# Kernel tuning notes

Measured on AMD Instinct MI355X. Metric: run time of the kernel, lower is better.

## Reference

```python
import jax, jax.numpy as jnp
import numpy as np

ZONEOUT = 0.15  # deterministic (eval-mode) zoneout on the output gate
HIDDEN = 128


def setup_inputs() -> dict:
    key = jax.random.key(0)
    k1, k2, k3, k4 = jax.random.split(key, 4)
    B, T, D, H = 512, 256, 256, HIDDEN
    x = jax.random.normal(k1, (B, T, D), dtype=jnp.float32)
    # gate projection for [i, f, o, g] gates, fan-in scaled
    Wx = jax.random.normal(k2, (4 * H, D), dtype=jnp.float32) / np.sqrt(D)
    Wh = jax.random.normal(k3, (4 * H, H), dtype=jnp.float32) / np.sqrt(H)
    b = jax.random.normal(k4, (4 * H,), dtype=jnp.float32) * 0.01
    return {"x": x, "Wx": Wx, "Wh": Wh, "b": b}


def reference(x, Wx, Wh, b):
    # x: [B, T, D]; returns (hids, cels, pogs) each [B, T, H]
    B, T, D = x.shape
    H = Wh.shape[1]
    z = jnp.asarray(ZONEOUT, dtype=x.dtype)

    def step(carry, xt):
        hid, cel, pog = carry  # each [B, H]
        gates = xt @ Wx.T + hid @ Wh.T + b  # [B, 4H]
        i_pre, f_pre, o_pre, g_pre = jnp.split(gates, 4, axis=-1)
        i = jax.nn.sigmoid(i_pre)
        f = jax.nn.sigmoid(f_pre)
        g = jnp.tanh(g_pre)
        # zoneout on the output gate: blend with previous output gate
        o = (1.0 - z) * jax.nn.sigmoid(o_pre) + z * pog
        cel_new = f * cel + i * g
        hid_new = o * jnp.tanh(cel_new)
        return (hid_new, cel_new, o), (hid_new, cel_new, o)

    zeros = jnp.zeros((B, H), dtype=x.dtype)
    xs = jnp.swapaxes(x, 0, 1)  # [T, B, D]
    _, (hids, cels, pogs) = jax.lax.scan(step, (zeros, zeros, zeros), xs)
    # [T, B, H] -> [B, T, H]
    return (jnp.swapaxes(hids, 0, 1), jnp.swapaxes(cels, 0, 1), jnp.swapaxes(pogs, 0, 1))
```

## Files before the change

### kernel.cpp

```cpp
#include <hip/hip_runtime.h>

typedef __attribute__((ext_vector_type(8))) short     bf16x8;
typedef __attribute__((ext_vector_type(4))) float     f32x4;

#define BSZ   512
#define TSZ   256
#define DSZ   256
#define HSZ   128
#define G4    512
#define OUT1  16777216L

__device__ inline unsigned short f2bf(float f) {
  union { float f; unsigned int u; } v; v.f = f;
  unsigned int r = (v.u + 0x7FFFu + ((v.u >> 16) & 1u)) >> 16;
  return (unsigned short)r;
}
__device__ inline float bf2f(unsigned int s) {
  union { unsigned int u; float f; } v; v.u = s << 16;
  return v.f;
}
__device__ inline float sig_fast(float x)  { return 1.0f / (1.0f + __expf(-x)); }
__device__ inline float tanh_fast(float x) { return 1.0f - 2.0f / (__expf(2.0f * x) + 1.0f); }

__global__ __launch_bounds__(512, 2)
void gemm_xw(const float* __restrict__ x, const float* __restrict__ Wx,
             const float* __restrict__ bias, unsigned short* __restrict__ xw) {
  __shared__ unsigned short aT[2][4096];

  const int tid = threadIdx.x;
  const int w   = tid >> 6;
  const int l   = tid & 63;
  const int p   = l & 15;
  const int r16 = l >> 4;
  const long m0blk = (long)blockIdx.x * 512;

  bf16x8 wf[4][8];
#pragma unroll
  for (int nt = 0; nt < 4; ++nt) {
#pragma unroll
    for (int c = 0; c < 8; ++c) {
      const float* src = Wx + (long)(w * 64 + nt * 16 + p) * DSZ + c * 32 + r16 * 8;
      float4 lo = *(const float4*)src;
      float4 hi = *(const float4*)(src + 4);
      bf16x8 f;
      f[0] = (short)f2bf(lo.x); f[1] = (short)f2bf(lo.y);
      f[2] = (short)f2bf(lo.z); f[3] = (short)f2bf(lo.w);
      f[4] = (short)f2bf(hi.x); f[5] = (short)f2bf(hi.y);
      f[6] = (short)f2bf(hi.z); f[7] = (short)f2bf(hi.w);
      wf[nt][c] = f;
    }
  }
  float bn[4];
#pragma unroll
  for (int nt = 0; nt < 4; ++nt) bn[nt] = bias[w * 64 + nt * 16 + p];

  const float* asrc = x + (m0blk + (l & 15)) * DSZ + (4 * w + r16) * 8;
  const int wl8 = (w * 64 + l) * 8;

  float4 va = *(const float4*)asrc;
  float4 vb = *(const float4*)(asrc + 4);
  asrc += 16 * DSZ;

  for (int i = 0; i < 32; ++i) {
    bf16x8 fr;
    fr[0] = (short)f2bf(va.x); fr[1] = (short)f2bf(va.y);
    fr[2] = (short)f2bf(va.z); fr[3] = (short)f2bf(va.w);
    fr[4] = (short)f2bf(vb.x); fr[5] = (short)f2bf(vb.y);
    fr[6] = (short)f2bf(vb.z); fr[7] = (short)f2bf(vb.w);
    *(bf16x8*)&aT[i & 1][wl8] = fr;

    if (i < 31) {
      va = *(const float4*)asrc;
      vb = *(const float4*)(asrc + 4);
      asrc += 16 * DSZ;
    }

    asm volatile("s_waitcnt lgkmcnt(0)" ::: "memory");
    __builtin_amdgcn_s_barrier();

    f32x4 acc[4];
#pragma unroll
    for (int nt = 0; nt < 4; ++nt)
      acc[nt] = (f32x4){bn[nt], bn[nt], bn[nt], bn[nt]};

#pragma unroll
    for (int c = 0; c < 8; ++c) {
      bf16x8 aF = *(const bf16x8*)&aT[i & 1][(c * 64 + l) * 8];
#pragma unroll
      for (int nt = 0; nt < 4; ++nt)
        acc[nt] = __builtin_amdgcn_mfma_f32_16x16x32_bf16(aF, wf[nt][c], acc[nt], 0, 0, 0);
    }

    const long rowbase = ((long)((i & 15) * 16 + r16 * 4) * BSZ + (blockIdx.x * 2 + (i >> 4))) * G4
                         + w * 64 + p;
#pragma unroll
    for (int r = 0; r < 4; ++r) {
      const long rb = rowbase + (long)r * (BSZ * G4);
#pragma unroll
      for (int nt = 0; nt < 4; ++nt)
        xw[rb + nt * 16] = f2bf(acc[nt][r]);
    }
  }
}

__global__ __launch_bounds__(512, 2)
void lstm_rec_mfma(const unsigned short* __restrict__ xw, const float* __restrict__ Wh,
                   float* __restrict__ outH, float* __restrict__ outC,
                   float* __restrict__ outP) {
  __shared__ unsigned short h_lds[2 * 2048];

  const int tid  = threadIdx.x;
  const int w    = tid >> 6;
  const int lane = tid & 63;
  const int p    = lane & 15;
  const int r16  = lane >> 4;
  const int b0   = blockIdx.x * 2;

  bf16x8 whF[4][4];
#pragma unroll
  for (int q = 0; q < 4; ++q) {
#pragma unroll
    for (int c = 0; c < 4; ++c) {
      const float* src = Wh + ((q * 128 + w * 16 + p) * HSZ + c * 32 + r16 * 8);
      float4 lo = *(const float4*)src;
      float4 hi = *(const float4*)(src + 4);
      bf16x8 f;
      f[0] = (short)f2bf(lo.x); f[1] = (short)f2bf(lo.y);
      f[2] = (short)f2bf(lo.z); f[3] = (short)f2bf(lo.w);
      f[4] = (short)f2bf(hi.x); f[5] = (short)f2bf(hi.y);
      f[6] = (short)f2bf(hi.z); f[7] = (short)f2bf(hi.w);
      whF[q][c] = f;
    }
  }

  for (int i = tid; i < 2 * 2048; i += 512) h_lds[i] = 0;

  float cel0 = 0.f, cel1 = 0.f, pog0 = 0.f, pog1 = 0.f;

  const int colw = w * 16 + p;
  const int c_  = colw >> 5, kk = colw & 31;
  const int lhi = (kk >> 3) << 4, jj = kk & 7;
  const int wr0 = c_ * 512 + (0 | lhi) * 8 + jj;
  const int wr1 = c_ * 512 + (1 | lhi) * 8 + jj;

  const unsigned short* xp = xw + (long)b0 * G4;
  const long XSTR = (long)BSZ * G4;

  unsigned int xvA[8], xvB[8];
#pragma unroll
  for (int q = 0; q < 4; ++q) {
    xvA[2 * q]     = xp[colw + q * 128];
    xvA[2 * q + 1] = xp[colw + G4 + q * 128];
  }
  xp += XSTR;

  float* pH0 = outH + (long)b0 * TSZ * HSZ;
  float* pC0 = outC + (long)b0 * TSZ * HSZ;
  float* pP0 = outP + (long)b0 * TSZ * HSZ;
  float* pH1 = pH0 + (long)TSZ * HSZ;
  float* pC1 = pC0 + (long)TSZ * HSZ;
  float* pP1 = pP0 + (long)TSZ * HSZ;

  f32x4 acc[4];
#pragma unroll
  for (int q = 0; q < 4; ++q) acc[q] = (f32x4){0.f, 0.f, 0.f, 0.f};

  __syncthreads();

#define STEP(RDOFF, WROFF, XC, XN, PREF)                                        \
  {                                                                             \
    bf16x8 aF[4];                                                               \
    _Pragma("unroll")                                                           \
    for (int c = 0; c < 4; ++c)                                                 \
      aF[c] = *(const bf16x8*)&h_lds[(RDOFF) + c * 512 + lane * 8];             \
    if (PREF) {                                                                 \
      _Pragma("unroll")                                                         \
      for (int q = 0; q < 4; ++q) {                                             \
        XN[2 * q]     = xp[colw + q * 128];                                     \
        XN[2 * q + 1] = xp[colw + G4 + q * 128];                                \
      }                                                                         \
      xp += XSTR;                                                               \
    }                                                                           \
    _Pragma("unroll")                                                           \
    for (int q = 0; q < 4; ++q) {                                               \
      acc[q][0] = bf2f(XC[2 * q]);                                              \
      acc[q][1] = bf2f(XC[2 * q + 1]);                                          \
    }                                                                           \
    _Pragma("unroll")                                                           \
    for (int q = 0; q < 4; ++q)                                                 \
      _Pragma("unroll")                                                         \
      for (int c = 0; c < 4; ++c)                                               \
        acc[q] = __builtin_amdgcn_mfma_f32_16x16x32_bf16(aF[c], whF[q][c], acc[q], 0, 0, 0); \
    float i0 = sig_fast(acc[0][0]), i1 = sig_fast(acc[0][1]);                   \
    float f0 = sig_fast(acc[1][0]), f1 = sig_fast(acc[1][1]);                   \
    float s0 = sig_fast(acc[2][0]), s1 = sig_fast(acc[2][1]);                   \
    float o0 = 0.85f * s0 + 0.15f * pog0, o1 = 0.85f * s1 + 0.15f * pog1;       \
    float g0 = tanh_fast(acc[3][0]), g1 = tanh_fast(acc[3][1]);                 \
    cel0 = f0 * cel0 + i0 * g0; cel1 = f1 * cel1 + i1 * g1;                     \
    float h0 = o0 * tanh_fast(cel0), h1 = o1 * tanh_fast(cel1);                 \
    pog0 = o0; pog1 = o1;                                                       \
    if (lane < 16) {                                                            \
      pH0[colw] = h0; pC0[colw] = cel0; pP0[colw] = o0;                         \
      pH1[colw] = h1; pC1[colw] = cel1; pP1[colw] = o1;                         \
      h_lds[(WROFF) + wr0] = f2bf(h0);                                          \
      h_lds[(WROFF) + wr1] = f2bf(h1);                                          \
    }                                                                           \
    pH0 += HSZ; pC0 += HSZ; pP0 += HSZ;                                         \
    pH1 += HSZ; pC1 += HSZ; pP1 += HSZ;                                         \
    asm volatile("s_waitcnt lgkmcnt(0)" ::: "memory");    \
    __builtin_amdgcn_s_barrier();                        \
  }

  for (int it = 0; it < 127; ++it) {
    STEP(0, 2048, xvA, xvB, true)
    STEP(2048, 0, xvB, xvA, true)
  }
  STEP(0, 2048, xvA, xvB, true)
  STEP(2048, 0, xvB, xvA, false)
#undef STEP
}

extern "C" void kernel_launch(void* const* d_in, const int* in_sizes, int n_in,
                              void* d_out, int out_size, void* d_ws, size_t ws_size,
                              hipStream_t stream) {
  const float* x    = (const float*)d_in[0];
  const float* Wx   = (const float*)d_in[1];
  const float* Wh   = (const float*)d_in[2];
  const float* bias = (const float*)d_in[3];

  float* outH = (float*)d_out;
  float* outC = outH + OUT1;
  float* outP = outC + OUT1;

  unsigned short* xwp = (unsigned short*)d_ws;

  dim3 g1(256), tb1(512);
  dim3 g2(256), tb2(512);

  gemm_xw<<<g1, tb1, 0, stream>>>(x, Wx, bias, xwp);
  lstm_rec_mfma<<<g2, tb2, 0, stream>>>(xwp, Wh, outH, outC, outP);
}
```

Measured before the change: 585.8 us.

## Process one batch row per recurrent block and interleave gate columns in xw

```diff
diff --git a/kernel.cpp b/kernel.cpp
--- a/kernel.cpp
+++ b/kernel.cpp
@@ -9,15 +9,18 @@
 #define HSZ   128
 #define G4    512
 #define OUT1  16777216L
+#define XSTR  262144L
 
 __device__ inline unsigned short f2bf(float f) {
   union { float f; unsigned int u; } v; v.f = f;
   unsigned int r = (v.u + 0x7FFFu + ((v.u >> 16) & 1u)) >> 16;
   return (unsigned short)r;
 }
-__device__ inline float bf2f(unsigned int s) {
-  union { unsigned int u; float f; } v; v.u = s << 16;
-  return v.f;
+__device__ inline float bf_lo(unsigned int u) {
+  union { unsigned int u; float f; } v; v.u = u << 16; return v.f;
+}
+__device__ inline float bf_hi(unsigned int u) {
+  union { unsigned int u; float f; } v; v.u = u & 0xFFFF0000u; return v.f;
 }
 __device__ inline float sig_fast(float x)  { return 1.0f / (1.0f + __expf(-x)); }
 __device__ inline float tanh_fast(float x) { return 1.0f - 2.0f / (__expf(2.0f * x) + 1.0f); }
@@ -91,19 +94,22 @@
         acc[nt] = __builtin_amdgcn_mfma_f32_16x16x32_bf16(aF, wf[nt][c], acc[nt], 0, 0, 0);
     }
 
-    const long rowbase = ((long)((i & 15) * 16 + r16 * 4) * BSZ + (blockIdx.x * 2 + (i >> 4))) * G4
-                         + w * 64 + p;
+    const int t0 = (i & 15) * 16 + r16 * 4;
+    const int bb = blockIdx.x * 2 + (i >> 4);
+    const int q  = w >> 1;
+    const int colw0 = (w & 1) * 64 + p;
+    const long base0 = (long)t0 * XSTR + (long)bb * G4 + colw0 * 4 + q;
 #pragma unroll
     for (int r = 0; r < 4; ++r) {
-      const long rb = rowbase + (long)r * (BSZ * G4);
+      const long rb = base0 + (long)r * XSTR;
 #pragma unroll
       for (int nt = 0; nt < 4; ++nt)
-        xw[rb + nt * 16] = f2bf(acc[nt][r]);
-    }
-  }
-}
-
-__global__ __launch_bounds__(512, 2)
+        xw[rb + nt * 64] = f2bf(acc[nt][r]);
+    }
+  }
+}
+
+__global__ __launch_bounds__(512, 4)
 void lstm_rec_mfma(const unsigned short* __restrict__ xw, const float* __restrict__ Wh,
                    float* __restrict__ outH, float* __restrict__ outC,
                    float* __restrict__ outP) {
@@ -114,7 +120,7 @@
   const int lane = tid & 63;
   const int p    = lane & 15;
   const int r16  = lane >> 4;
-  const int b0   = blockIdx.x * 2;
+  const int b    = blockIdx.x;
 
   bf16x8 whF[4][4];
 #pragma unroll
@@ -135,31 +141,22 @@
 
   for (int i = tid; i < 2 * 2048; i += 512) h_lds[i] = 0;
 
-  float cel0 = 0.f, cel1 = 0.f, pog0 = 0.f, pog1 = 0.f;
+  float cel0 = 0.f, pog0 = 0.f;
 
   const int colw = w * 16 + p;
   const int c_  = colw >> 5, kk = colw & 31;
   const int lhi = (kk >> 3) << 4, jj = kk & 7;
-  const int wr0 = c_ * 512 + (0 | lhi) * 8 + jj;
-  const int wr1 = c_ * 512 + (1 | lhi) * 8 + jj;
-
-  const unsigned short* xp = xw + (long)b0 * G4;
-  const long XSTR = (long)BSZ * G4;
-
-  unsigned int xvA[8], xvB[8];
-#pragma unroll
-  for (int q = 0; q < 4; ++q) {
-    xvA[2 * q]     = xp[colw + q * 128];
-    xvA[2 * q + 1] = xp[colw + G4 + q * 128];
-  }
-  xp += XSTR;
-
-  float* pH0 = outH + (long)b0 * TSZ * HSZ;
-  float* pC0 = outC + (long)b0 * TSZ * HSZ;
-  float* pP0 = outP + (long)b0 * TSZ * HSZ;
-  float* pH1 = pH0 + (long)TSZ * HSZ;
-  float* pC1 = pC0 + (long)TSZ * HSZ;
-  float* pP1 = pP0 + (long)TSZ * HSZ;
+  const int wr0 = c_ * 512 + lhi * 8 + jj;
+
+  const unsigned short* xb = xw + (long)b * G4 + colw * 4;
+
+  uint2 xv0 = *(const uint2*)(xb);
+  uint2 xv1 = *(const uint2*)(xb + XSTR);
+  const unsigned short* xpn = xb + 2 * XSTR;
+
+  float* pH = outH + (long)b * TSZ * HSZ;
+  float* pC = outC + (long)b * TSZ * HSZ;
+  float* pP = outP + (long)b * TSZ * HSZ;
 
   f32x4 acc[4];
 #pragma unroll
@@ -167,56 +164,43 @@
 
   __syncthreads();
 
-#define STEP(RDOFF, WROFF, XC, XN, PREF)                                        \
+#define STEP(RDOFF, WROFF, XV, PREF)                                            \
   {                                                                             \
     bf16x8 aF[4];                                                               \
     _Pragma("unroll")                                                           \
     for (int c = 0; c < 4; ++c)                                                 \
       aF[c] = *(const bf16x8*)&h_lds[(RDOFF) + c * 512 + lane * 8];             \
-    if (PREF) {                                                                 \
-      _Pragma("unroll")                                                         \
-      for (int q = 0; q < 4; ++q) {                                             \
-        XN[2 * q]     = xp[colw + q * 128];                                     \
-        XN[2 * q + 1] = xp[colw + G4 + q * 128];                                \
-      }                                                                         \
-      xp += XSTR;                                                               \
-    }                                                                           \
-    _Pragma("unroll")                                                           \
-    for (int q = 0; q < 4; ++q) {                                               \
-      acc[q][0] = bf2f(XC[2 * q]);                                              \
-      acc[q][1] = bf2f(XC[2 * q + 1]);                                          \
-    }                                                                           \
+                    \
+    acc[0][0] = bf_lo(XV.x);  acc[1][0] = bf_hi(XV.x);                          \
+    acc[2][0] = bf_lo(XV.y);  acc[3][0] = bf_hi(XV.y);                          \
+    if (PREF) { XV = *(const uint2*)xpn; xpn += XSTR; }                         \
     _Pragma("unroll")                                                           \
     for (int q = 0; q < 4; ++q)                                                 \
       _Pragma("unroll")                                                         \
       for (int c = 0; c < 4; ++c)                                               \
         acc[q] = __builtin_amdgcn_mfma_f32_16x16x32_bf16(aF[c], whF[q][c], acc[q], 0, 0, 0); \
-    float i0 = sig_fast(acc[0][0]), i1 = sig_fast(acc[0][1]);                   \
-    float f0 = sig_fast(acc[1][0]), f1 = sig_fast(acc[1][1]);                   \
-    float s0 = sig_fast(acc[2][0]), s1 = sig_fast(acc[2][1]);                   \
-    float o0 = 0.85f * s0 + 0.15f * pog0, o1 = 0.85f * s1 + 0.15f * pog1;       \
-    float g0 = tanh_fast(acc[3][0]), g1 = tanh_fast(acc[3][1]);                 \
-    cel0 = f0 * cel0 + i0 * g0; cel1 = f1 * cel1 + i1 * g1;                     \
-    float h0 = o0 * tanh_fast(cel0), h1 = o1 * tanh_fast(cel1);                 \
-    pog0 = o0; pog1 = o1;                                                       \
+    float i0 = sig_fast(acc[0][0]);                                             \
+    float f0 = sig_fast(acc[1][0]);                                             \
+    float o0 = 0.85f * sig_fast(acc[2][0]) + 0.15f * pog0;                      \
+    float g0 = tanh_fast(acc[3][0]);                                            \
+    cel0 = f0 * cel0 + i0 * g0;                                                 \
+    float h0 = o0 * tanh_fast(cel0);                                            \
+    pog0 = o0;                                                                  \
     if (lane < 16) {                                                            \
-      pH0[colw] = h0; pC0[colw] = cel0; pP0[colw] = o0;                         \
-      pH1[colw] = h1; pC1[colw] = cel1; pP1[colw] = o1;                         \
+      pH[colw] = h0; pC[colw] = cel0; pP[colw] = o0;                            \
       h_lds[(WROFF) + wr0] = f2bf(h0);                                          \
-      h_lds[(WROFF) + wr1] = f2bf(h1);                                          \
     }                                                                           \
-    pH0 += HSZ; pC0 += HSZ; pP0 += HSZ;                                         \
-    pH1 += HSZ; pC1 += HSZ; pP1 += HSZ;                                         \
+    pH += HSZ; pC += HSZ; pP += HSZ;                                            \
     asm volatile("s_waitcnt lgkmcnt(0)" ::: "memory");    \
     __builtin_amdgcn_s_barrier();                        \
   }
 
   for (int it = 0; it < 127; ++it) {
-    STEP(0, 2048, xvA, xvB, true)
-    STEP(2048, 0, xvB, xvA, true)
-  }
-  STEP(0, 2048, xvA, xvB, true)
-  STEP(2048, 0, xvB, xvA, false)
+    STEP(0, 2048, xv0, true)
+    STEP(2048, 0, xv1, true)
+  }
+  STEP(0, 2048, xv0, false)
+  STEP(2048, 0, xv1, false)
 #undef STEP
 }
 
@@ -235,7 +219,7 @@
   unsigned short* xwp = (unsigned short*)d_ws;
 
   dim3 g1(256), tb1(512);
-  dim3 g2(256), tb2(512);
+  dim3 g2(512), tb2(512);
 
   gemm_xw<<<g1, tb1, 0, stream>>>(x, Wx, bias, xwp);
   lstm_rec_mfma<<<g2, tb2, 0, stream>>>(xwp, Wh, outH, outC, outP);
```

After: 636.4 us. 1.09x slower.
